# Kernel tuning notes

Hardware: AMD Instinct MI355X
Metric: run time of the kernel (lower is better)

Reference implementation:

```python
import jax, jax.numpy as jnp
import numpy as np

NUM_GRAPHS = 256
N_NODES = 128          # nodes per graph (equal-size graphs)
DEG = 16               # average degree
NUM_EDGES = NUM_GRAPHS * N_NODES * DEG
NUM_HEADS = 8
SCALE = 10.0
INF_REPLACE = 1.0


def setup_inputs() -> dict:
    key = jax.random.key(0)
    k1, k2, k3 = jax.random.split(key, 3)
    # each graph owns a contiguous block of N_NODES global node ids
    eg = jnp.repeat(jnp.arange(NUM_GRAPHS, dtype=jnp.int32), N_NODES * DEG)
    src_loc = jax.random.randint(k1, (NUM_EDGES,), 0, N_NODES, dtype=jnp.int32)
    dst_loc = jax.random.randint(k2, (NUM_EDGES,), 0, N_NODES, dtype=jnp.int32)
    edge_index = jnp.stack([eg * N_NODES + src_loc, eg * N_NODES + dst_loc])  # [2, E]
    edge_weight = jax.random.uniform(k3, (NUM_EDGES,), minval=0.1, maxval=1.0)
    batch = jnp.repeat(jnp.arange(NUM_GRAPHS, dtype=jnp.int32), N_NODES)  # [N_total]
    return {
        'edge_index': edge_index,
        'edge_weight': edge_weight,
        'batch': batch,
        'num_graphs': NUM_GRAPHS,
        'max_num_nodes': N_NODES,
    }


def _shortest_path_bias(edge_index, edge_weight, batch, num_graphs, max_num_nodes):
    G, n = num_graphs, max_num_nodes
    inf = jnp.inf
    # per-graph node offsets (graphs occupy contiguous node-id blocks)
    counts = jnp.bincount(batch, length=G)
    offsets = jnp.concatenate([jnp.zeros((1,), counts.dtype), jnp.cumsum(counts)[:-1]])
    src, dst = edge_index[0], edge_index[1]
    eg = batch[src]                              # graph id of each edge
    u = src - offsets[eg]                        # local node ids
    v = dst - offsets[eg]
    # self-loops are skipped in the original (masked to +inf -> no-op under min)
    w = jnp.where(src == dst, inf, edge_weight)

    # init dense distance: inf off-diagonal, 0 on diagonal, edge weights scattered
    dist = jnp.full((G, n, n), inf, dtype=edge_weight.dtype)
    diag = jnp.arange(n)
    dist = dist.at[:, diag, diag].set(0.0)
    dist = dist.at[eg, u, v].min(w)

    # batched Floyd-Warshall: d[i,j] = min(d[i,j], d[i,k] + d[k,j]) for all graphs
    def body(d, k):
        col = jax.lax.dynamic_slice_in_dim(d, k, 1, axis=2)  # [G, n, 1] = d[:, :, k]
        row = jax.lax.dynamic_slice_in_dim(d, k, 1, axis=1)  # [G, 1, n] = d[:, k, :]
        return jnp.minimum(d, col + row), None
    dist, _ = jax.lax.scan(body, dist, jnp.arange(n))

    # replace unreachable with 2 * max finite distance (per graph)
    finite = jnp.isfinite(dist)
    fmax = jnp.max(jnp.where(finite, dist, -inf), axis=(1, 2), keepdims=True)
    unreach = jnp.where(jnp.isfinite(fmax), 2.0 * fmax, INF_REPLACE)
    dist = jnp.where(finite, dist, unreach)

    # normalize per graph and scale
    max_val = jnp.maximum(jnp.max(dist, axis=(1, 2), keepdims=True), 1e-8)
    bias = -SCALE * (dist / max_val)
    bias = jnp.nan_to_num(bias, nan=0.0, posinf=-1e6, neginf=-1e6)

    # expand over heads and flatten to [B*H, n, n]
    bias = jnp.broadcast_to(bias[:, None], (G, NUM_HEADS, n, n))
    return bias.reshape(G * NUM_HEADS, n, n)


def reference(edge_index, edge_weight, batch, num_graphs, max_num_nodes):
    return _shortest_path_bias(edge_index, edge_weight, batch, num_graphs, max_num_nodes)
```

## Files before the change

### kernel.cpp

```cpp
#include <hip/hip_runtime.h>

#define NHEADS 8
#define NN     128
#define NCELL  (NN * NN)
#define NT     512
#define SCALE_F 10.0f

#define RP_O 0
#define RP_N 2048
#define CP_O 4096
#define CP_N 6144
#define DP   8192
#define DPT  8448
#define RED  8704

template<int CB>
__device__ __forceinline__ void block_step(float (&dd)[4][8], float* lds,
                                           const int kb, const int t,
                                           const int rgrp, const int cgrp)
{
    if ((rgrp >> 2) == kb) {
        const int q = rgrp & 3;
        #pragma unroll
        for (int rr = 0; rr < 4; ++rr) {
            const int iloc = 4 * q + rr;
            const int sw = iloc & 7;
            #pragma unroll
            for (int c = 0; c < 2; ++c) {
                float4 v = make_float4(dd[rr][c*4+0], dd[rr][c*4+1],
                                       dd[rr][c*4+2], dd[rr][c*4+3]);
                *reinterpret_cast<float4*>(
                    &lds[RP_O + iloc*128 + (((cgrp + 16*c) ^ sw) << 2)]) = v;
            }
        }
    }
    {
        const int q2 = (cgrp - 4 * kb) & 15;
        if (q2 < 4) {
            #pragma unroll
            for (int e = 0; e < 4; ++e) {
                const int jj = 4 * q2 + e;
                float4 v = make_float4(dd[0][CB+e], dd[1][CB+e],
                                       dd[2][CB+e], dd[3][CB+e]);
                *reinterpret_cast<float4*>(
                    &lds[CP_O + jj*128 + ((rgrp ^ (jj & 7)) << 2)]) = v;
            }
        }
    }

    if ((t >> 6) == kb) {
        const int l  = t & 63;
        const int ra = l >> 4;
        const int ca = ((l & 15) - 4 * kb) & 15;
        const bool act = (ca < 4);
        #pragma unroll
        for (int k = 0; k < 16; ++k) {
            const int kq = k >> 2, ke = k & 3;
            const int lsc = (l & 48) | ((4 * kb + kq) & 15);
            const int lsr = (kq << 4) | (l & 15);
            float cv0 = __shfl(dd[0][CB+ke], lsc);
            float cv1 = __shfl(dd[1][CB+ke], lsc);
            float cv2 = __shfl(dd[2][CB+ke], lsc);
            float cv3 = __shfl(dd[3][CB+ke], lsc);
            float rv0 = __shfl(dd[ke][CB+0], lsr);
            float rv1 = __shfl(dd[ke][CB+1], lsr);
            float rv2 = __shfl(dd[ke][CB+2], lsr);
            float rv3 = __shfl(dd[ke][CB+3], lsr);
            if (act) {
                dd[0][CB+0]=fminf(dd[0][CB+0],cv0+rv0); dd[0][CB+1]=fminf(dd[0][CB+1],cv0+rv1);
                dd[0][CB+2]=fminf(dd[0][CB+2],cv0+rv2); dd[0][CB+3]=fminf(dd[0][CB+3],cv0+rv3);
                dd[1][CB+0]=fminf(dd[1][CB+0],cv1+rv0); dd[1][CB+1]=fminf(dd[1][CB+1],cv1+rv1);
                dd[1][CB+2]=fminf(dd[1][CB+2],cv1+rv2); dd[1][CB+3]=fminf(dd[1][CB+3],cv1+rv3);
                dd[2][CB+0]=fminf(dd[2][CB+0],cv2+rv0); dd[2][CB+1]=fminf(dd[2][CB+1],cv2+rv1);
                dd[2][CB+2]=fminf(dd[2][CB+2],cv2+rv2); dd[2][CB+3]=fminf(dd[2][CB+3],cv2+rv3);
                dd[3][CB+0]=fminf(dd[3][CB+0],cv3+rv0); dd[3][CB+1]=fminf(dd[3][CB+1],cv3+rv1);
                dd[3][CB+2]=fminf(dd[3][CB+2],cv3+rv2); dd[3][CB+3]=fminf(dd[3][CB+3],cv3+rv3);
            }
        }
        if (act) {
            #pragma unroll
            for (int rr = 0; rr < 4; ++rr) {
                float4 v = make_float4(dd[rr][CB+0], dd[rr][CB+1],
                                       dd[rr][CB+2], dd[rr][CB+3]);
                *reinterpret_cast<float4*>(&lds[DP + (4*ra+rr)*16 + 4*ca]) = v;
            }
            #pragma unroll
            for (int e = 0; e < 4; ++e) {
                float4 v = make_float4(dd[0][CB+e], dd[1][CB+e],
                                       dd[2][CB+e], dd[3][CB+e]);
                *reinterpret_cast<float4*>(&lds[DPT + (4*ca+e)*16 + 4*ra]) = v;
            }
        }
    }
    __syncthreads();

    {
        const int a  = t >> 5;
        const int ch = t & 31;
        float da[16], dc[16];
        #pragma unroll
        for (int c = 0; c < 4; ++c) {
            float4 v1 = *reinterpret_cast<const float4*>(&lds[DP  + a*16 + 4*c]);
            float4 v2 = *reinterpret_cast<const float4*>(&lds[DPT + a*16 + 4*c]);
            da[4*c+0]=v1.x; da[4*c+1]=v1.y; da[4*c+2]=v1.z; da[4*c+3]=v1.w;
            dc[4*c+0]=v2.x; dc[4*c+1]=v2.y; dc[4*c+2]=v2.z; dc[4*c+3]=v2.w;
        }
        const float INF = __builtin_huge_valf();
        float aR0=INF,aR1=INF,aR2=INF,aR3=INF, aC0=INF,aC1=INF,aC2=INF,aC3=INF;
        #pragma unroll
        for (int k = 0; k < 16; ++k) {
            const int off = k*128 + (((ch) ^ (k & 7)) << 2);
            float4 r4 = *reinterpret_cast<const float4*>(&lds[RP_O + off]);
            float4 c4 = *reinterpret_cast<const float4*>(&lds[CP_O + off]);
            aR0 = fminf(aR0, da[k] + r4.x); aR1 = fminf(aR1, da[k] + r4.y);
            aR2 = fminf(aR2, da[k] + r4.z); aR3 = fminf(aR3, da[k] + r4.w);
            aC0 = fminf(aC0, dc[k] + c4.x); aC1 = fminf(aC1, dc[k] + c4.y);
            aC2 = fminf(aC2, dc[k] + c4.z); aC3 = fminf(aC3, dc[k] + c4.w);
        }
        const int offo = a*128 + ((ch ^ (a & 7)) << 2);
        *reinterpret_cast<float4*>(&lds[RP_N + offo]) = make_float4(aR0,aR1,aR2,aR3);
        *reinterpret_cast<float4*>(&lds[CP_N + offo]) = make_float4(aC0,aC1,aC2,aC3);
    }
    __syncthreads();

    #pragma unroll
    for (int kp = 0; kp < 8; ++kp) {
        const int k0 = 2*kp, k1 = 2*kp + 1;
        float4 cp0 = *reinterpret_cast<const float4*>(&lds[CP_N + k0*128 + ((rgrp       ^ (k0&7)) << 2)]);
        float4 r0a = *reinterpret_cast<const float4*>(&lds[RP_N + k0*128 + ((cgrp       ^ (k0&7)) << 2)]);
        float4 r0b = *reinterpret_cast<const float4*>(&lds[RP_N + k0*128 + (((cgrp+16)  ^ (k0&7)) << 2)]);
        float4 cp1 = *reinterpret_cast<const float4*>(&lds[CP_N + k1*128 + ((rgrp       ^ (k1&7)) << 2)]);
        float4 r1a = *reinterpret_cast<const float4*>(&lds[RP_N + k1*128 + ((cgrp       ^ (k1&7)) << 2)]);
        float4 r1b = *reinterpret_cast<const float4*>(&lds[RP_N + k1*128 + (((cgrp+16)  ^ (k1&7)) << 2)]);
        const float c0[4] = {cp0.x, cp0.y, cp0.z, cp0.w};
        const float c1[4] = {cp1.x, cp1.y, cp1.z, cp1.w};
        const float ra0[4] = {r0a.x, r0a.y, r0a.z, r0a.w};
        const float rb0[4] = {r0b.x, r0b.y, r0b.z, r0b.w};
        const float ra1[4] = {r1a.x, r1a.y, r1a.z, r1a.w};
        const float rb1[4] = {r1b.x, r1b.y, r1b.z, r1b.w};
        #pragma unroll
        for (int rr = 0; rr < 4; ++rr) {
            #pragma unroll
            for (int e = 0; e < 4; ++e) {
                dd[rr][e]   = fminf(fminf(dd[rr][e],   c0[rr] + ra0[e]), c1[rr] + ra1[e]);
                dd[rr][4+e] = fminf(fminf(dd[rr][4+e], c0[rr] + rb0[e]), c1[rr] + rb1[e]);
            }
        }
    }
}

__global__ __launch_bounds__(NT)
void spb_fw_kernel(const int* __restrict__ edge_index,
                   const float* __restrict__ edge_weight,
                   const int num_edges, const int epg,
                   float* __restrict__ out)
{
    __shared__ float lds[NCELL];
    const float INF = __builtin_huge_valf();
    const int t    = threadIdx.x;
    const int g    = blockIdx.x;
    const int cgrp = t & 15;
    const int rgrp = t >> 4;

    #pragma unroll
    for (int c = 0; c < 8; ++c) {
        const int m   = t + (c << 9);
        const int i   = m >> 5;
        const int scm = m & 31;
        const int c0  = (scm ^ (i & 7)) << 2;
        float4 v;
        v.x = (c0 + 0 == i) ? 0.0f : INF;
        v.y = (c0 + 1 == i) ? 0.0f : INF;
        v.z = (c0 + 2 == i) ? 0.0f : INF;
        v.w = (c0 + 3 == i) ? 0.0f : INF;
        *reinterpret_cast<float4*>(&lds[m << 2]) = v;
    }
    __syncthreads();

    const int ebase = g * epg;
    for (int e = t; e < epg; e += NT) {
        const int idx = ebase + e;
        const int src = edge_index[idx];
        const int dst = edge_index[num_edges + idx];
        const float w = edge_weight[idx];
        const int u = src - g * NN;
        const int v = dst - g * NN;
        if (u != v && (unsigned)u < (unsigned)NN && (unsigned)v < (unsigned)NN) {
            const int a = (u << 7) + (v ^ ((u & 7) << 2));
            atomicMin(reinterpret_cast<int*>(&lds[a]), __float_as_int(w));
        }
    }
    __syncthreads();

    float dd[4][8];
    #pragma unroll
    for (int rr = 0; rr < 4; ++rr) {
        const int i = (rgrp << 2) + rr;
        const int s = i & 7;
        #pragma unroll
        for (int c = 0; c < 2; ++c) {
            float4 v = *reinterpret_cast<const float4*>(
                &lds[(i << 7) + (((cgrp + 16*c) ^ s) << 2)]);
            dd[rr][c*4+0]=v.x; dd[rr][c*4+1]=v.y; dd[rr][c*4+2]=v.z; dd[rr][c*4+3]=v.w;
        }
    }
    __syncthreads();

    #pragma unroll
    for (int kbl = 0; kbl < 4; ++kbl)
        block_step<0>(dd, lds, kbl, t, rgrp, cgrp);
    #pragma unroll
    for (int kbl = 0; kbl < 4; ++kbl)
        block_step<4>(dd, lds, 4 + kbl, t, rgrp, cgrp);

    float mF = 0.0f, mA = 0.0f;
    #pragma unroll
    for (int rr = 0; rr < 4; ++rr)
        #pragma unroll
        for (int j = 0; j < 8; ++j) {
            const float v = dd[rr][j];
            mA = fmaxf(mA, v);
            mF = fmaxf(mF, v < INF ? v : 0.0f);
        }
    #pragma unroll
    for (int o = 32; o > 0; o >>= 1) {
        mF = fmaxf(mF, __shfl_xor(mF, o));
        mA = fmaxf(mA, __shfl_xor(mA, o));
    }
    if ((t & 63) == 0) {
        lds[RED + ((t >> 6) << 1)]     = mF;
        lds[RED + ((t >> 6) << 1) + 1] = mA;
    }
    __syncthreads();
    mF = lds[RED]; mA = lds[RED + 1];
    #pragma unroll
    for (int wv = 1; wv < 8; ++wv) {
        mF = fmaxf(mF, lds[RED + wv*2]);
        mA = fmaxf(mA, lds[RED + wv*2 + 1]);
    }
    const float twoF  = 2.0f * mF;
    const float maxv  = fmaxf((mA == INF) ? twoF : mF, 1e-8f);
    const float nscal = -SCALE_F / maxv;

    float* const outg = out + (size_t)g * (NHEADS * NCELL);
    #pragma unroll
    for (int rr = 0; rr < 4; ++rr) {
        const int i = (rgrp << 2) + rr;
        #pragma unroll
        for (int c = 0; c < 2; ++c) {
            float4 v;
            v.x = ((dd[rr][c*4+0] == INF) ? twoF : dd[rr][c*4+0]) * nscal;
            v.y = ((dd[rr][c*4+1] == INF) ? twoF : dd[rr][c*4+1]) * nscal;
            v.z = ((dd[rr][c*4+2] == INF) ? twoF : dd[rr][c*4+2]) * nscal;
            v.w = ((dd[rr][c*4+3] == INF) ? twoF : dd[rr][c*4+3]) * nscal;
            const int o = (i << 7) + (cgrp << 2) + (c << 6);
            #pragma unroll
            for (int h = 0; h < NHEADS; ++h) {
                *reinterpret_cast<float4*>(&outg[h * NCELL + o]) = v;
            }
        }
    }
}

extern "C" void kernel_launch(void* const* d_in, const int* in_sizes, int n_in,
                              void* d_out, int out_size, void* d_ws, size_t ws_size,
                              hipStream_t stream)
{
    const int*   edge_index  = (const int*)d_in[0];
    const float* edge_w      = (const float*)d_in[1];
    const int E    = in_sizes[1];
    const int Ntot = in_sizes[2];
    const int G    = Ntot / NN;
    const int epg  = E / G;
    float* out = (float*)d_out;
    spb_fw_kernel<<<G, NT, 0, stream>>>(edge_index, edge_w, E, epg, out);
}
```

Measured before the change: 74.72 us.

## Rework diagonal FW block via LDS+readlane, rebalance panel phase, nontemporal output stores

```diff
diff --git a/kernel.cpp b/kernel.cpp
--- a/kernel.cpp
+++ b/kernel.cpp
@@ -5,6 +5,8 @@
 #define NCELL  (NN * NN)
 #define NT     512
 #define SCALE_F 10.0f
+
+typedef float nfloat4 __attribute__((ext_vector_type(4)));
 
 #define RP_O 0
 #define RP_N 2048
@@ -19,6 +21,8 @@
                                            const int kb, const int t,
                                            const int rgrp, const int cgrp)
 {
+    const float INF = __builtin_huge_valf();
+
     if ((rgrp >> 2) == kb) {
         const int q = rgrp & 3;
         #pragma unroll
@@ -49,91 +53,94 @@
     }
 
     if ((t >> 6) == kb) {
-        const int l  = t & 63;
-        const int ra = l >> 4;
-        const int ca = ((l & 15) - 4 * kb) & 15;
-        const bool act = (ca < 4);
+        const int l = t & 63;
+        const int p = cgrp - 4 * (kb & 3);
+        if ((unsigned)p < 4u) {
+            const int q = rgrp & 3;
+            #pragma unroll
+            for (int rr = 0; rr < 4; ++rr) {
+                *reinterpret_cast<float4*>(&lds[DP + (4*q+rr)*16 + 4*p]) =
+                    make_float4(dd[rr][CB+0], dd[rr][CB+1], dd[rr][CB+2], dd[rr][CB+3]);
+            }
+        }
+        asm volatile("s_waitcnt lgkmcnt(0)" ::: "memory");
+        float T[16];
+        const int lr = l & 15;
+        #pragma unroll
+        for (int c4 = 0; c4 < 4; ++c4) {
+            float4 v = *reinterpret_cast<const float4*>(&lds[DP + lr*16 + 4*c4]);
+            T[c4*4+0]=v.x; T[c4*4+1]=v.y; T[c4*4+2]=v.z; T[c4*4+3]=v.w;
+        }
         #pragma unroll
         for (int k = 0; k < 16; ++k) {
-            const int kq = k >> 2, ke = k & 3;
-            const int lsc = (l & 48) | ((4 * kb + kq) & 15);
-            const int lsr = (kq << 4) | (l & 15);
-            float cv0 = __shfl(dd[0][CB+ke], lsc);
-            float cv1 = __shfl(dd[1][CB+ke], lsc);
-            float cv2 = __shfl(dd[2][CB+ke], lsc);
-            float cv3 = __shfl(dd[3][CB+ke], lsc);
-            float rv0 = __shfl(dd[ke][CB+0], lsr);
-            float rv1 = __shfl(dd[ke][CB+1], lsr);
-            float rv2 = __shfl(dd[ke][CB+2], lsr);
-            float rv3 = __shfl(dd[ke][CB+3], lsr);
-            if (act) {
-                dd[0][CB+0]=fminf(dd[0][CB+0],cv0+rv0); dd[0][CB+1]=fminf(dd[0][CB+1],cv0+rv1);
-                dd[0][CB+2]=fminf(dd[0][CB+2],cv0+rv2); dd[0][CB+3]=fminf(dd[0][CB+3],cv0+rv3);
-                dd[1][CB+0]=fminf(dd[1][CB+0],cv1+rv0); dd[1][CB+1]=fminf(dd[1][CB+1],cv1+rv1);
-                dd[1][CB+2]=fminf(dd[1][CB+2],cv1+rv2); dd[1][CB+3]=fminf(dd[1][CB+3],cv1+rv3);
-                dd[2][CB+0]=fminf(dd[2][CB+0],cv2+rv0); dd[2][CB+1]=fminf(dd[2][CB+1],cv2+rv1);
-                dd[2][CB+2]=fminf(dd[2][CB+2],cv2+rv2); dd[2][CB+3]=fminf(dd[2][CB+3],cv2+rv3);
-                dd[3][CB+0]=fminf(dd[3][CB+0],cv3+rv0); dd[3][CB+1]=fminf(dd[3][CB+1],cv3+rv1);
-                dd[3][CB+2]=fminf(dd[3][CB+2],cv3+rv2); dd[3][CB+3]=fminf(dd[3][CB+3],cv3+rv3);
-            }
-        }
-        if (act) {
-            #pragma unroll
-            for (int rr = 0; rr < 4; ++rr) {
-                float4 v = make_float4(dd[rr][CB+0], dd[rr][CB+1],
-                                       dd[rr][CB+2], dd[rr][CB+3]);
-                *reinterpret_cast<float4*>(&lds[DP + (4*ra+rr)*16 + 4*ca]) = v;
-            }
-            #pragma unroll
-            for (int e = 0; e < 4; ++e) {
-                float4 v = make_float4(dd[0][CB+e], dd[1][CB+e],
-                                       dd[2][CB+e], dd[3][CB+e]);
-                *reinterpret_cast<float4*>(&lds[DPT + (4*ca+e)*16 + 4*ra]) = v;
-            }
+            float rk[16];
+            #pragma unroll
+            for (int j = 0; j < 16; ++j)
+                rk[j] = __int_as_float(
+                    __builtin_amdgcn_readlane(__float_as_int(T[j]), k));
+            const float dik = T[k];
+            #pragma unroll
+            for (int j = 0; j < 16; ++j)
+                T[j] = fminf(T[j], dik + rk[j]);
+        }
+        if (l < 16) {
+            #pragma unroll
+            for (int c4 = 0; c4 < 4; ++c4)
+                *reinterpret_cast<float4*>(&lds[DP + l*16 + 4*c4]) =
+                    make_float4(T[c4*4], T[c4*4+1], T[c4*4+2], T[c4*4+3]);
+            #pragma unroll
+            for (int j = 0; j < 16; ++j)
+                lds[DPT + j*16 + l] = T[j];
         }
     }
     __syncthreads();
 
     {
-        const int a  = t >> 5;
+        const int ap = t >> 6;
         const int ch = t & 31;
-        float da[16], dc[16];
-        #pragma unroll
-        for (int c = 0; c < 4; ++c) {
-            float4 v1 = *reinterpret_cast<const float4*>(&lds[DP  + a*16 + 4*c]);
-            float4 v2 = *reinterpret_cast<const float4*>(&lds[DPT + a*16 + 4*c]);
-            da[4*c+0]=v1.x; da[4*c+1]=v1.y; da[4*c+2]=v1.z; da[4*c+3]=v1.w;
-            dc[4*c+0]=v2.x; dc[4*c+1]=v2.y; dc[4*c+2]=v2.z; dc[4*c+3]=v2.w;
-        }
-        const float INF = __builtin_huge_valf();
-        float aR0=INF,aR1=INF,aR2=INF,aR3=INF, aC0=INF,aC1=INF,aC2=INF,aC3=INF;
+        const int isC   = (t >> 5) & 1;
+        const int base  = isC ? CP_O : RP_O;
+        const int dbase = isC ? DPT  : DP;
+        const int obase = isC ? CP_N : RP_N;
+        float d0[16], d1[16];
+        #pragma unroll
+        for (int c4 = 0; c4 < 4; ++c4) {
+            float4 v0 = *reinterpret_cast<const float4*>(&lds[dbase + (2*ap  )*16 + 4*c4]);
+            float4 v1 = *reinterpret_cast<const float4*>(&lds[dbase + (2*ap+1)*16 + 4*c4]);
+            d0[c4*4+0]=v0.x; d0[c4*4+1]=v0.y; d0[c4*4+2]=v0.z; d0[c4*4+3]=v0.w;
+            d1[c4*4+0]=v1.x; d1[c4*4+1]=v1.y; d1[c4*4+2]=v1.z; d1[c4*4+3]=v1.w;
+        }
+        float a00=INF,a01=INF,a02=INF,a03=INF;
+        float a10=INF,a11=INF,a12=INF,a13=INF;
         #pragma unroll
         for (int k = 0; k < 16; ++k) {
-            const int off = k*128 + (((ch) ^ (k & 7)) << 2);
-            float4 r4 = *reinterpret_cast<const float4*>(&lds[RP_O + off]);
-            float4 c4 = *reinterpret_cast<const float4*>(&lds[CP_O + off]);
-            aR0 = fminf(aR0, da[k] + r4.x); aR1 = fminf(aR1, da[k] + r4.y);
-            aR2 = fminf(aR2, da[k] + r4.z); aR3 = fminf(aR3, da[k] + r4.w);
-            aC0 = fminf(aC0, dc[k] + c4.x); aC1 = fminf(aC1, dc[k] + c4.y);
-            aC2 = fminf(aC2, dc[k] + c4.z); aC3 = fminf(aC3, dc[k] + c4.w);
-        }
-        const int offo = a*128 + ((ch ^ (a & 7)) << 2);
-        *reinterpret_cast<float4*>(&lds[RP_N + offo]) = make_float4(aR0,aR1,aR2,aR3);
-        *reinterpret_cast<float4*>(&lds[CP_N + offo]) = make_float4(aC0,aC1,aC2,aC3);
+            float4 r = *reinterpret_cast<const float4*>(
+                &lds[base + k*128 + ((ch ^ (k & 7)) << 2)]);
+            a00=fminf(a00,d0[k]+r.x); a01=fminf(a01,d0[k]+r.y);
+            a02=fminf(a02,d0[k]+r.z); a03=fminf(a03,d0[k]+r.w);
+            a10=fminf(a10,d1[k]+r.x); a11=fminf(a11,d1[k]+r.y);
+            a12=fminf(a12,d1[k]+r.z); a13=fminf(a13,d1[k]+r.w);
+        }
+        *reinterpret_cast<float4*>(
+            &lds[obase + (2*ap  )*128 + ((ch ^ ((2*ap  ) & 7)) << 2)]) =
+            make_float4(a00,a01,a02,a03);
+        *reinterpret_cast<float4*>(
+            &lds[obase + (2*ap+1)*128 + ((ch ^ ((2*ap+1) & 7)) << 2)]) =
+            make_float4(a10,a11,a12,a13);
     }
     __syncthreads();
 
     #pragma unroll
     for (int kp = 0; kp < 8; ++kp) {
         const int k0 = 2*kp, k1 = 2*kp + 1;
-        float4 cp0 = *reinterpret_cast<const float4*>(&lds[CP_N + k0*128 + ((rgrp       ^ (k0&7)) << 2)]);
-        float4 r0a = *reinterpret_cast<const float4*>(&lds[RP_N + k0*128 + ((cgrp       ^ (k0&7)) << 2)]);
-        float4 r0b = *reinterpret_cast<const float4*>(&lds[RP_N + k0*128 + (((cgrp+16)  ^ (k0&7)) << 2)]);
-        float4 cp1 = *reinterpret_cast<const float4*>(&lds[CP_N + k1*128 + ((rgrp       ^ (k1&7)) << 2)]);
-        float4 r1a = *reinterpret_cast<const float4*>(&lds[RP_N + k1*128 + ((cgrp       ^ (k1&7)) << 2)]);
-        float4 r1b = *reinterpret_cast<const float4*>(&lds[RP_N + k1*128 + (((cgrp+16)  ^ (k1&7)) << 2)]);
-        const float c0[4] = {cp0.x, cp0.y, cp0.z, cp0.w};
-        const float c1[4] = {cp1.x, cp1.y, cp1.z, cp1.w};
+        float4 cp0 = *reinterpret_cast<const float4*>(&lds[CP_N + k0*128 + ((rgrp      ^ (k0&7)) << 2)]);
+        float4 r0a = *reinterpret_cast<const float4*>(&lds[RP_N + k0*128 + ((cgrp      ^ (k0&7)) << 2)]);
+        float4 r0b = *reinterpret_cast<const float4*>(&lds[RP_N + k0*128 + (((cgrp+16) ^ (k0&7)) << 2)]);
+        float4 cp1 = *reinterpret_cast<const float4*>(&lds[CP_N + k1*128 + ((rgrp      ^ (k1&7)) << 2)]);
+        float4 r1a = *reinterpret_cast<const float4*>(&lds[RP_N + k1*128 + ((cgrp      ^ (k1&7)) << 2)]);
+        float4 r1b = *reinterpret_cast<const float4*>(&lds[RP_N + k1*128 + (((cgrp+16) ^ (k1&7)) << 2)]);
+        const float c0[4]  = {cp0.x, cp0.y, cp0.z, cp0.w};
+        const float c1[4]  = {cp1.x, cp1.y, cp1.z, cp1.w};
         const float ra0[4] = {r0a.x, r0a.y, r0a.z, r0a.w};
         const float rb0[4] = {r0b.x, r0b.y, r0b.z, r0b.w};
         const float ra1[4] = {r1a.x, r1a.y, r1a.z, r1a.w};
@@ -248,7 +255,7 @@
         const int i = (rgrp << 2) + rr;
         #pragma unroll
         for (int c = 0; c < 2; ++c) {
-            float4 v;
+            nfloat4 v;
             v.x = ((dd[rr][c*4+0] == INF) ? twoF : dd[rr][c*4+0]) * nscal;
             v.y = ((dd[rr][c*4+1] == INF) ? twoF : dd[rr][c*4+1]) * nscal;
             v.z = ((dd[rr][c*4+2] == INF) ? twoF : dd[rr][c*4+2]) * nscal;
@@ -256,7 +263,8 @@
             const int o = (i << 7) + (cgrp << 2) + (c << 6);
             #pragma unroll
             for (int h = 0; h < NHEADS; ++h) {
-                *reinterpret_cast<float4*>(&outg[h * NCELL + o]) = v;
+                __builtin_nontemporal_store(
+                    v, reinterpret_cast<nfloat4*>(&outg[h * NCELL + o]));
             }
         }
     }
```

After: 68.80 us. -7.9%, faster.
